# Kernel tuning notes

Measured on AMD Instinct MI355X. Metric: run time of the kernel, lower is better.

Reference implementation:

```python
import jax, jax.numpy as jnp
import numpy as np

B, C = 1024, 256
GRID_H, GRID_W, PAD_H, PAD_W = 11, 15, 13, 17  # 165 hexes, padded 13x17

def _build_convinds():
    off0 = np.array([-17, -16, -1, 0, 1, 17, 18])
    off1 = np.array([-18, -17, -1, 0, 1, 16, 17])
    inds = np.zeros((GRID_H, GRID_W, 7), dtype=np.int32)
    for y in range(1, GRID_H + 1):
        for x in range(1, GRID_W + 1):
            off = off0 if y % 2 == 0 else off1
            inds[y - 1, x - 1] = off + (y * PAD_W + x)
    return jnp.asarray(inds.reshape(-1))  # (165*7,)

CONVINDS = _build_convinds()

def hexconv(x, W, b):
    # x: (B, 165, C); W: (7C, C); b: (C,)
    bsz = x.shape[0]
    c = x.shape[-1]
    padded = jnp.zeros((bsz, PAD_H, PAD_W, c), x.dtype)
    padded = padded.at[:, 1:1 + GRID_H, 1:1 + GRID_W, :].set(x.reshape(bsz, GRID_H, GRID_W, c))
    padded = padded.reshape(bsz, PAD_H * PAD_W, c)
    gathered = padded[:, CONVINDS, :].reshape(bsz, GRID_H * GRID_W, 7 * c)  # (B,165,7C)
    return gathered @ W + b

def leaky(v):
    return jax.nn.leaky_relu(v, negative_slope=0.01)

def setup_inputs() -> dict:
    key = jax.random.key(0)
    k1, k2, k3, k4, k5 = jax.random.split(key, 5)
    scale = 1.0 / np.sqrt(7 * C)
    return {
        "x": jax.random.normal(k1, (B, 165, C), dtype=jnp.float32),
        "W1": jax.random.uniform(k2, (7 * C, C), jnp.float32, -scale, scale),
        "b1": jax.random.uniform(k3, (C,), jnp.float32, -scale, scale),
        "W2": jax.random.uniform(k4, (7 * C, C), jnp.float32, -scale, scale),
        "b2": jax.random.uniform(k5, (C,), jnp.float32, -scale, scale),
    }

def reference(x, W1, b1, W2, b2):
    # depth=1 residual block: x = act(conv2(act(conv1(x))) + x)
    h = leaky(hexconv(x, W1, b1))
    return leaky(hexconv(h, W2, b2) + x)
```

## Files before the change

kernel.cpp:

```cpp
#include <hip/hip_runtime.h>

typedef __attribute__((ext_vector_type(8))) short short8;
typedef __attribute__((ext_vector_type(4))) float f32x4;

typedef __attribute__((address_space(1))) const unsigned int guint;
typedef __attribute__((address_space(3))) unsigned int luint;

__device__ __forceinline__ void gload16(const void* g, void* l) {
    __builtin_amdgcn_global_load_lds((guint*)g, (luint*)l, 16, 0, 0);
}

__device__ __forceinline__ unsigned short f2bf(float f) {
    unsigned u = __float_as_uint(f);
    u += 0x7fffu + ((u >> 16) & 1u);
    return (unsigned short)(u >> 16);
}
__device__ __forceinline__ float bf2f(unsigned short s) {
    return __uint_as_float((unsigned)s << 16);
}

__device__ const int g_DY[7]  = {-1, -1, 0, 0, 0, 1, 1};
__device__ const int g_DXO[7] = { 0,  1, -1, 0, 1, 0, 1};
__device__ const int g_DXE[7] = {-1,  0, -1, 0, 1, -1, 0};

__global__ void __launch_bounds__(256) cvt_x_kernel(const float* __restrict__ in,
                                                    unsigned short* __restrict__ out,
                                                    int n8) {
    int stride = gridDim.x * blockDim.x;
    for (int i = blockIdx.x * blockDim.x + threadIdx.x; i < n8; i += stride) {
        const float4* p = reinterpret_cast<const float4*>(in) + (size_t)i * 2;
        float4 a = p[0], b = p[1];
        short8 o;
        o[0] = (short)f2bf(a.x); o[1] = (short)f2bf(a.y);
        o[2] = (short)f2bf(a.z); o[3] = (short)f2bf(a.w);
        o[4] = (short)f2bf(b.x); o[5] = (short)f2bf(b.y);
        o[6] = (short)f2bf(b.z); o[7] = (short)f2bf(b.w);
        *reinterpret_cast<short8*>(out + (size_t)i * 8) = o;
    }
}

__global__ void __launch_bounds__(256) cvt_wt_kernel(const float* __restrict__ W1,
                                                     const float* __restrict__ W2,
                                                     unsigned short* __restrict__ W1t,
                                                     unsigned short* __restrict__ W2t) {
    const float* W = blockIdx.z ? W2 : W1;
    unsigned short* Wt = blockIdx.z ? W2t : W1t;
    int k0 = blockIdx.x * 64;
    int n0 = blockIdx.y * 64;
    __shared__ float tile[64][65];
    for (int e = threadIdx.x; e < 4096; e += 256) {
        int r = e >> 6, c = e & 63;
        tile[r][c] = W[(size_t)(k0 + r) * 256 + n0 + c];
    }
    __syncthreads();
    for (int e = threadIdx.x; e < 4096; e += 256) {
        int r = e >> 6, c = e & 63;
        Wt[(size_t)(n0 + r) * 1792 + k0 + c] = f2bf(tile[c][r]);
    }
}

template <int MODE>
__global__ void __launch_bounds__(512, 2) hexconv8_kernel(
        const unsigned short* __restrict__ xg,
        const unsigned short* __restrict__ wt,
        const float* __restrict__ bias,
        const unsigned short* __restrict__ residbf,
        void* __restrict__ outp,
        const unsigned short* __restrict__ zp)
{
    __shared__ unsigned short smem[65536];

    const int t = threadIdx.x;
    const int lane = t & 63, w = t >> 6;
    const int wr = w >> 2, wc = w & 3;

    int bid = blockIdx.x;
    int xcd = bid & 7, idx = bid >> 3;
    const int mb = (xcd < 4 ? xcd * 83 : 332 + (xcd - 4) * 82) + idx;

    const int trow = t >> 3;
    const int chunk = t & 7;
    const int aswz = (chunk ^ (trow & 7)) * 8;
    int yv[4], xv[4], brow[4], aoff[4];
    const unsigned short* wsrcp[4];
#pragma unroll
    for (int i = 0; i < 4; ++i) {
        int row = i * 64 + trow;
        int m = mb * 256 + row;
        int b = m / 165;
        int ii = m - b * 165;
        int y = ii / 15;
        int x = ii - y * 15;
        yv[i] = y; xv[i] = x; brow[i] = m - ii;
        wsrcp[i] = wt + (size_t)row * 1792 + aswz;
    }

#define CALC_AOFF(J) do {                                                     \
        int dy_ = g_DY[J];                                                    \
        int dxo_ = g_DXO[J], dxe_ = g_DXE[J];                                 \
        _Pragma("unroll")                                                     \
        for (int i = 0; i < 4; ++i) {                                         \
            int dx_ = (yv[i] & 1) ? dxo_ : dxe_;                              \
            int ny_ = yv[i] + dy_, nx_ = xv[i] + dx_;                         \
            bool v_ = ((unsigned)ny_ < 11u) && ((unsigned)nx_ < 15u);         \
            aoff[i] = v_ ? ((brow[i] + ny_ * 15 + nx_) * 256 + aswz) : -1;    \
        } } while (0)

    int offA[4][2], offB[2][2][2];
    {
        int l15 = lane & 15, lhi = lane >> 4, l7 = lane & 7;
#pragma unroll
        for (int f = 0; f < 4; ++f)
#pragma unroll
            for (int ks = 0; ks < 2; ++ks)
                offA[f][ks] = (wr * 128 + f * 16 + l15) * 64 + (((ks * 4 + lhi) ^ l7) * 8);
#pragma unroll
        for (int nh = 0; nh < 2; ++nh)
#pragma unroll
            for (int g = 0; g < 2; ++g)
#pragma unroll
                for (int ks = 0; ks < 2; ++ks)
                    offB[nh][g][ks] = (wc * 64 + nh * 32 + g * 16 + l15) * 64 +
                                      (((ks * 4 + lhi) ^ l7) * 8);
    }

    f32x4 acc[8][4];
#pragma unroll
    for (int mf = 0; mf < 8; ++mf)
#pragma unroll
        for (int nf = 0; nf < 4; ++nf) {
            f32x4 z = {0.f, 0.f, 0.f, 0.f};
            acc[mf][nf] = z;
        }
    short8 a[4][2], b0[2][2], b1[2][2];

#define STAGE_A(TT, P) do {                                                   \
        int c0_ = ((TT) & 3) * 64;                                            \
        _Pragma("unroll")                                                     \
        for (int i = 0; i < 4; ++i) {                                         \
            const unsigned short* g_ = (aoff[i] >= 0) ? (xg + aoff[i] + c0_) : zp; \
            gload16(g_, &smem[(P) * 32768 + i * 4096 + t * 8]);               \
        } } while (0)
#define STAGE_B(TT, P) do {                                                   \
        int ko_ = (TT) * 64;                                                  \
        _Pragma("unroll")                                                     \
        for (int i = 0; i < 4; ++i)                                           \
            gload16(wsrcp[i] + ko_, &smem[(P) * 32768 + 16384 + i * 4096 + t * 8]); \
        } while (0)

#define LDA(P, MH) do { _Pragma("unroll") for (int f = 0; f < 4; ++f)         \
        _Pragma("unroll") for (int ks = 0; ks < 2; ++ks)                      \
            a[f][ks] = *(const short8*)&smem[(P) * 32768 + (MH) * 4096 + offA[f][ks]]; \
        } while (0)
#define LDB(P, NH, DST) do { _Pragma("unroll") for (int g = 0; g < 2; ++g)    \
        _Pragma("unroll") for (int ks = 0; ks < 2; ++ks)                      \
            DST[g][ks] = *(const short8*)&smem[(P) * 32768 + 16384 + offB[NH][g][ks]]; \
        } while (0)

#define QUAD(MH, NH, BF) do { _Pragma("unroll") for (int f = 0; f < 4; ++f)   \
        _Pragma("unroll") for (int g = 0; g < 2; ++g)                         \
        _Pragma("unroll") for (int ks = 0; ks < 2; ++ks)                      \
            acc[(MH) * 4 + f][(NH) * 2 + g] = __builtin_amdgcn_mfma_f32_16x16x32_bf16( \
                a[f][ks], BF[g][ks], acc[(MH) * 4 + f][(NH) * 2 + g], 0, 0, 0); \
        } while (0)

#define BAR() __builtin_amdgcn_s_barrier()
#define LGKM0() do { asm volatile("s_waitcnt lgkmcnt(0)" ::: "memory");       \
                     __builtin_amdgcn_sched_barrier(0); } while (0)
#define VM0() asm volatile("s_waitcnt vmcnt(0)" ::: "memory")
#define PRIO(N) __builtin_amdgcn_s_setprio(N)

#define TILE(T28, P) do {                                                     \
        int tt_ = (T28) + 1;                                                  \
                                                                      \
        if (tt_ < 28) {                                                       \
            if ((tt_ & 3) == 0) { int jn_ = tt_ >> 2; CALC_AOFF(jn_); }       \
            STAGE_A(tt_, 1 - (P));                                            \
        }                                                                     \
        LDA(P, 0); LDB(P, 0, b0);                                             \
        BAR(); LGKM0(); PRIO(1); QUAD(0, 0, b0); PRIO(0); BAR();              \
                                                                      \
        if (tt_ < 28) STAGE_B(tt_, 1 - (P));                                  \
        LDB(P, 1, b1);                                                        \
        BAR(); LGKM0(); PRIO(1); QUAD(0, 1, b1); PRIO(0); BAR();              \
                                                                      \
        LDA(P, 1);                                                            \
        BAR(); LGKM0(); PRIO(1); QUAD(1, 1, b1); PRIO(0); BAR();              \
                                                                      \
        PRIO(1); QUAD(1, 0, b0); PRIO(0);                                     \
        VM0(); BAR();                                                         \
    } while (0)

    CALC_AOFF(0);
    STAGE_A(0, 0);
    STAGE_B(0, 0);
    VM0(); BAR();

#pragma unroll 1
    for (int it = 0; it < 14; ++it) {
        TILE(2 * it, 0);
        TILE(2 * it + 1, 1);
    }

    const size_t mrowbase = (size_t)mb * 256 + wr * 128;
    const int l15 = lane & 15, lq = (lane >> 4) * 4;
    if (MODE == 0) {
        unsigned short* outh = (unsigned short*)outp;
#pragma unroll
        for (int nf = 0; nf < 4; ++nf) {
            int col = wc * 64 + nf * 16 + l15;
            float bb = bias[col];
#pragma unroll
            for (int mf = 0; mf < 8; ++mf)
#pragma unroll
                for (int r = 0; r < 4; ++r) {
                    size_t mr = mrowbase + mf * 16 + lq + r;
                    float v = acc[mf][nf][r] + bb;
                    v = v > 0.f ? v : 0.01f * v;
                    outh[mr * 256 + col] = f2bf(v);
                }
        }
    } else {
        float* outf = (float*)outp;
#pragma unroll
        for (int nf = 0; nf < 4; ++nf) {
            int col = wc * 64 + nf * 16 + l15;
            float bb = bias[col];
#pragma unroll
            for (int mf = 0; mf < 8; ++mf)
#pragma unroll
                for (int r = 0; r < 4; ++r) {
                    size_t mr = mrowbase + mf * 16 + lq + r;
                    float v = acc[mf][nf][r] + bb + bf2f(residbf[mr * 256 + col]);
                    v = v > 0.f ? v : 0.01f * v;
                    outf[mr * 256 + col] = v;
                }
        }
    }
}

extern "C" void kernel_launch(void* const* d_in, const int* in_sizes, int n_in,
                              void* d_out, int out_size, void* d_ws, size_t ws_size,
                              hipStream_t stream) {
    const float* x  = (const float*)d_in[0];
    const float* W1 = (const float*)d_in[1];
    const float* b1 = (const float*)d_in[2];
    const float* W2 = (const float*)d_in[3];
    const float* b2 = (const float*)d_in[4];
    float* out = (float*)d_out;

    const size_t XBF = (size_t)1024 * 165 * 256 * 2;
    const size_t WTB = (size_t)256 * 1792 * 2;
    char* ws = (char*)d_ws;
    unsigned short* zp  = (unsigned short*)ws;
    unsigned short* xbf = (unsigned short*)(ws + 256);
    unsigned short* hbf = (unsigned short*)(ws + 256 + XBF);
    unsigned short* w1t = (unsigned short*)(ws + 256 + 2 * XBF);
    unsigned short* w2t = (unsigned short*)(ws + 256 + 2 * XBF + WTB);

    hipMemsetAsync(d_ws, 0, 256, stream);
    cvt_x_kernel<<<2048, 256, 0, stream>>>(x, xbf, 5406720);
    cvt_wt_kernel<<<dim3(28, 4, 2), 256, 0, stream>>>(W1, W2, w1t, w2t);
    hexconv8_kernel<0><<<660, 512, 0, stream>>>(xbf, w1t, b1, nullptr, (void*)hbf, zp);
    hexconv8_kernel<1><<<660, 512, 0, stream>>>(hbf, w2t, b2, xbf, (void*)out, zp);
}
```

Before: 450.6 us.

## Split A-tile staging and use partial vmcnt waits to overlap loads

Prefetch of the next K-tile is reordered: all B-tile loads and half of the A-tile rows are issued first, and the remaining A rows are issued after the first MFMA quadrant. The full vmcnt(0) drain at the end of each tile is replaced by partial waits (vmcnt 8 mid-tile, vmcnt 2 at the end). This lets the last global-to-LDS copies stay in flight across the tile boundary, with completion enforced just before the A half that needs them is read. It relies on the A-row-to-half mapping and the in-order vmcnt counting being right; if either is off, the kernel would read stale LDS data.

```diff
diff --git a/kernel.cpp b/kernel.cpp
--- a/kernel.cpp
+++ b/kernel.cpp
@@ -134,18 +134,13 @@
         }
     short8 a[4][2], b0[2][2], b1[2][2];
 
-#define STAGE_A(TT, P) do {                                                   \
-        int c0_ = ((TT) & 3) * 64;                                            \
-        _Pragma("unroll")                                                     \
-        for (int i = 0; i < 4; ++i) {                                         \
-            const unsigned short* g_ = (aoff[i] >= 0) ? (xg + aoff[i] + c0_) : zp; \
-            gload16(g_, &smem[(P) * 32768 + i * 4096 + t * 8]);               \
-        } } while (0)
-#define STAGE_B(TT, P) do {                                                   \
-        int ko_ = (TT) * 64;                                                  \
+#define STAGE_A_ONE(I, TT, Q) do { int c0_ = ((TT) & 3) * 64;                 \
+        const unsigned short* g_ = (aoff[I] >= 0) ? (xg + aoff[I] + c0_) : zp; \
+        gload16(g_, &smem[(Q) * 32768 + (I) * 4096 + t * 8]); } while (0)
+#define STAGE_B_ALL(TT, Q) do { int ko_ = (TT) * 64;                          \
         _Pragma("unroll")                                                     \
         for (int i = 0; i < 4; ++i)                                           \
-            gload16(wsrcp[i] + ko_, &smem[(P) * 32768 + 16384 + i * 4096 + t * 8]); \
+            gload16(wsrcp[i] + ko_, &smem[(Q) * 32768 + 16384 + i * 4096 + t * 8]); \
         } while (0)
 
 #define LDA(P, MH) do { _Pragma("unroll") for (int f = 0; f < 4; ++f)         \
@@ -167,34 +162,45 @@
 #define BAR() __builtin_amdgcn_s_barrier()
 #define LGKM0() do { asm volatile("s_waitcnt lgkmcnt(0)" ::: "memory");       \
                      __builtin_amdgcn_sched_barrier(0); } while (0)
-#define VM0() asm volatile("s_waitcnt vmcnt(0)" ::: "memory")
+#define VMCNT(N) do { asm volatile("s_waitcnt vmcnt(" #N ")" ::: "memory");   \
+                      __builtin_amdgcn_sched_barrier(0); } while (0)
 #define PRIO(N) __builtin_amdgcn_s_setprio(N)
 
 #define TILE(T28, P) do {                                                     \
         int tt_ = (T28) + 1;                                                  \
-                                                                      \
-        if (tt_ < 28) {                                                       \
-            if ((tt_ & 3) == 0) { int jn_ = tt_ >> 2; CALC_AOFF(jn_); }       \
-            STAGE_A(tt_, 1 - (P));                                            \
+        bool st_ = (tt_ < 28);                                                \
+                          \
+        if (st_) {                                                            \
+            if ((tt_ & 3) == 0) CALC_AOFF(tt_ >> 2);                          \
+            STAGE_B_ALL(tt_, 1 - (P));                                        \
+            STAGE_A_ONE(0, tt_, 1 - (P));                                     \
+            STAGE_A_ONE(2, tt_, 1 - (P));                                     \
         }                                                                     \
         LDA(P, 0); LDB(P, 0, b0);                                             \
         BAR(); LGKM0(); PRIO(1); QUAD(0, 0, b0); PRIO(0); BAR();              \
-                                                                      \
-        if (tt_ < 28) STAGE_B(tt_, 1 - (P));                                  \
+                                   \
+        if (st_) {                                                            \
+            STAGE_A_ONE(1, tt_, 1 - (P));                                     \
+            STAGE_A_ONE(3, tt_, 1 - (P));                                     \
+        }                                                                     \
         LDB(P, 1, b1);                                                        \
-        BAR(); LGKM0(); PRIO(1); QUAD(0, 1, b1); PRIO(0); BAR();              \
+        BAR(); LGKM0(); PRIO(1); QUAD(0, 1, b1); PRIO(0);                     \
+        if (st_) { VMCNT(8); } else { VMCNT(0); }       \
+        BAR();                                                                \
                                                                       \
         LDA(P, 1);                                                            \
         BAR(); LGKM0(); PRIO(1); QUAD(1, 1, b1); PRIO(0); BAR();              \
                                                                       \
         PRIO(1); QUAD(1, 0, b0); PRIO(0);                                     \
-        VM0(); BAR();                                                         \
+        if (st_) { VMCNT(2); } else { VMCNT(0); }       \
+        BAR();                                                                \
     } while (0)
 
     CALC_AOFF(0);
-    STAGE_A(0, 0);
-    STAGE_B(0, 0);
-    VM0(); BAR();
+    STAGE_B_ALL(0, 0);
+    STAGE_A_ONE(0, 0, 0); STAGE_A_ONE(2, 0, 0);
+    STAGE_A_ONE(1, 0, 0); STAGE_A_ONE(3, 0, 0);
+    VMCNT(0); BAR();
 
 #pragma unroll 1
     for (int it = 0; it < 14; ++it) {
```

Result: no change. 458.6 us (+1.8%).
